# Optimization experiments

Hardware: AMD Instinct MI355X
Metric: run time of the kernel (lower is better)

The kernel has to match this reference:

```python
import jax, jax.numpy as jnp
import numpy as np

SELECTED_CLASS = 1  # matches init_kwargs


def _edt_sq(mask):
    """Exact squared Euclidean distance of each pixel to the nearest False pixel.
    Matches scipy.ndimage.distance_transform_edt(mask)**2 (2-pass separable,
    column scan + exact row-wise parabola minimization done brute-force in chunks).
    mask: (H, W) bool.
    """
    H, W = mask.shape
    BIG = np.float32(H + W)  # > any possible true distance, safe sentinel
    g = np.where(mask, BIG, np.float32(0.0)).astype(np.float32)
    for i in range(1, H):
        np.minimum(g[i], g[i - 1] + 1, out=g[i])
    for i in range(H - 2, -1, -1):
        np.minimum(g[i], g[i + 1] + 1, out=g[i])
    g2 = g * g  # (H, W) squared column distances
    k = np.arange(W, dtype=np.float32)
    d2 = np.empty((H, W), np.float32)
    CH = 64  # chunk of output columns to bound temp memory
    for j0 in range(0, W, CH):
        j = k[j0:j0 + CH]
        diff2 = (j[None, :] - k[:, None]) ** 2  # (W, Jc)
        d2[:, j0:j0 + CH] = (g2[:, :, None] + diff2[None]).min(axis=1)
    return d2


def _inner_boundary(mask):
    """skimage.segmentation.find_boundaries(mask, mode='inner'), connectivity=1:
    foreground pixels with at least one in-image 4-neighbor in background."""
    p = np.pad(mask, 1, constant_values=True)
    ero = p[1:-1, :-2] & p[1:-1, 2:] & p[:-2, 1:-1] & p[2:, 1:-1] & mask
    return mask & ~ero


def compute_sdf_np(y_true_sel):
    """Normalized signed distance map, faithful to BoundaryLoss.compute_sdf.
    y_true_sel: (B, 1, H, W) float; returns (B, 1, H, W) float32 in [-1, 1]."""
    masks = y_true_sel[:, 0].astype(bool)
    B, H, W = masks.shape
    out = np.zeros((B, 1, H, W), np.float32)
    for b in range(B):
        m = masks[b]
        if not m.any():
            continue  # original leaves zeros
        posdis = np.sqrt(_edt_sq(m))
        negdis = np.sqrt(_edt_sq(~m))
        sdf = (negdis - negdis.min()) / (negdis.max() - negdis.min()) \
            - (posdis - posdis.min()) / (posdis.max() - posdis.min())
        sdf[_inner_boundary(m)] = 0.0
        out[b, 0] = sdf
    return out


def setup_inputs():
    key = jax.random.key(0)
    k1, k2 = jax.random.split(key)
    B, C, H, W = 8, 4, 512, 512
    y_pred = jax.random.normal(k1, (B, C, H, W), dtype=jnp.float32)
    y_true = jax.random.randint(k2, (B, C, H, W), 0, 2).astype(jnp.float32)
    return {"y_pred": y_pred, "y_true": y_true}


def reference(y_pred, y_true):
    sel = SELECTED_CLASS
    # GT signed distance map (host-side, non-differentiable, as in the original
    # which round-trips through scipy on CPU): shape (B, 1, H, W)
    gt_sdf = jnp.asarray(compute_sdf_np(np.asarray(y_true[:, sel:sel + 1])))
    pc = jax.nn.sigmoid(y_pred)  # (B, C, H, W)
    # torch.einsum('bchw,bchw->bchw', pc, dc) with dc having c=1 broadcasts over C
    mult = pc * gt_sdf
    return mult.mean(axis=(1, 2, 3)).mean()
```

## Files before the change

### kernel.cpp

```cpp
#include <hip/hip_runtime.h>
#include <math.h>

#define B 8
#define C 4
#define H 512
#define W 512
#define SEL 1
#define BIGI 1024
#define NPIX (B*H*W)
#define CH 64
#define RC 8
#define TC 32
#define NSEG 16
#define LL 4
#define CINF 3000
#define G 8
#define NRU (B*H/G)
#define LOG2E 1.4426950408889634f

__global__ __launch_bounds__(512) void col_two_level(const float* __restrict__ ytrue,
                                                     unsigned short* __restrict__ gpkT,
                                                     unsigned* __restrict__ sumsD,
                                                     unsigned* __restrict__ sumsU) {
    __shared__ int sP[NSEG][TC + 1], sN[NSEG][TC + 1];
    __shared__ int sCP[NSEG][TC + 1], sCN[NSEG][TC + 1];

    int blk = blockIdx.x;
    int b   = blk >> 7;
    int rem = blk & 127;
    int jt  = rem >> 3;
    int rc  = rem & 7;
    int tid = threadIdx.x;
    int tx  = tid & (TC - 1);
    int ty  = tid >> 5;
    int j   = jt * TC + tx;
    int i0  = rc * CH + ty * LL;

    const float* m = ytrue + ((size_t)b * C + SEL) * H * W + j;
    int gfp[LL], gfn[LL];
    int pp = BIGI, pn = BIGI;
    #pragma unroll
    for (int r = 0; r < LL; ++r) {
        bool fg = (m[(size_t)(i0 + r) * W] != 0.0f);
        int vp = fg ? BIGI : 0;
        int vn = fg ? 0 : BIGI;
        vp = min(vp, pp + 1); gfp[r] = vp; pp = vp;
        vn = min(vn, pn + 1); gfn[r] = vn; pn = vn;
    }
    sP[ty][tx] = pp - ty * LL;
    sN[ty][tx] = pn - ty * LL;
    __syncthreads();

    int col = tid >> 4, seg = tid & 15;
    int wp = sP[seg][col], wn = sN[seg][col];
    #pragma unroll
    for (int d = 1; d < NSEG; d <<= 1) {
        int a1 = __shfl_up(wp, d, 16);
        int a2 = __shfl_up(wn, d, 16);
        if (seg >= d) { wp = min(wp, a1); wn = min(wn, a2); }
    }
    if (seg < NSEG - 1) {
        sCP[seg + 1][col] = seg * LL + wp;
        sCN[seg + 1][col] = seg * LL + wn;
    } else {
        int jj = jt * TC + col;
        sumsD[((size_t)(b * RC + rc)) * W + jj] =
            (unsigned)(seg * LL + wp) | ((unsigned)(seg * LL + wn) << 16);
    }
    if (seg == 0) { sCP[0][col] = BIGI; sCN[0][col] = BIGI; }
    __syncthreads();

    int cp = sCP[ty][tx], cn = sCN[ty][tx];
    int lbp = 1 << 20, lbn = 1 << 20;
    #pragma unroll
    for (int r = 0; r < LL; ++r) {
        int vp = min(gfp[r], cp + 1 + r); gfp[r] = vp; lbp = min(lbp, vp + r);
        int vn = min(gfn[r], cn + 1 + r); gfn[r] = vn; lbn = min(lbn, vn + r);
    }
    sP[ty][tx] = lbp + ty * LL;
    sN[ty][tx] = lbn + ty * LL;
    __syncthreads();

    int w2p = sP[seg][col], w2n = sN[seg][col];
    #pragma unroll
    for (int d = 1; d < NSEG; d <<= 1) {
        int a1 = __shfl_down(w2p, d, 16);
        int a2 = __shfl_down(w2n, d, 16);
        if (seg + d < NSEG) { w2p = min(w2p, a1); w2n = min(w2n, a2); }
    }
    if (seg > 0) {
        sCP[seg - 1][col] = w2p - seg * LL;
        sCN[seg - 1][col] = w2n - seg * LL;
    } else {
        int jj = jt * TC + col;
        sumsU[((size_t)(b * RC + rc)) * W + jj] =
            (unsigned)w2p | ((unsigned)w2n << 16);
    }
    if (seg == NSEG - 1) { sCP[NSEG - 1][col] = BIGI; sCN[NSEG - 1][col] = BIGI; }
    __syncthreads();

    int pbp = sCP[ty][tx], pbn = sCN[ty][tx];
    unsigned short g4[LL];
    #pragma unroll
    for (int r = LL - 1; r >= 0; --r) {
        int vp = min(gfp[r], pbp + 1); pbp = vp;
        int vn = min(gfn[r], pbn + 1); pbn = vn;
        int fg = (vn == 0) ? 1 : 0;
        int g2 = vp + vn;
        g4[r] = (unsigned short)((g2 << 1) | fg);
    }
    ushort4 pk; pk.x = g4[0]; pk.y = g4[1]; pk.z = g4[2]; pk.w = g4[3];
    *(ushort4*)(gpkT + (((size_t)b * (H / 4) + (i0 >> 2)) * W + j) * 4) = pk;
}

__global__ __launch_bounds__(512) void row_fused(const unsigned short* __restrict__ gpkT,
                                                 const unsigned* __restrict__ sumsD,
                                                 const unsigned* __restrict__ sumsU,
                                                 const float* __restrict__ ypred,
                                                 float* __restrict__ rowpart) {
    __shared__ float s1[G][W];
    __shared__ float sw[4][8];

    int blk = blockIdx.x;
    int b = blk >> 6;
    int g = blk & 63;
    int i0 = g * G;
    int rc = i0 >> 6;
    int j = threadIdx.x;

    const unsigned* sd = sumsD + (size_t)b * RC * W + j;
    const unsigned* su = sumsU + (size_t)b * RC * W + j;
    int Ap = CINF, An = CINF, Bp = CINF, Bn = CINF;
    #pragma unroll
    for (int q = 0; q < RC; ++q) {
        if (q < rc) {
            unsigned dv = sd[(size_t)q * W];
            int e = q * CH + CH - 1;
            Ap = min(Ap, (int)(dv & 0xFFFFu) - e);
            An = min(An, (int)(dv >> 16) - e);
        } else if (q > rc) {
            unsigned uv = su[(size_t)q * W];
            int s0 = q * CH;
            Bp = min(Bp, (int)(uv & 0xFFFFu) + s0);
            Bn = min(Bn, (int)(uv >> 16) + s0);
        }
    }

    float svr[G];
    #pragma unroll
    for (int h = 0; h < G; h += 4) {
        const ushort4 v4 = *(const ushort4*)(gpkT + (((size_t)b * (H / 4) + ((i0 + h) >> 2)) * W + j) * 4);
        unsigned short vv[4] = { v4.x, v4.y, v4.z, v4.w };
        #pragma unroll
        for (int r = 0; r < 4; ++r) {
            int ii = i0 + h + r;
            unsigned v = vv[r];
            int fg = v & 1;
            int gv = v >> 1;
            int gp = fg ? gv : 0;
            int gn = fg ? 0 : gv;
            gp = min(gp, min(Ap + ii, Bp - ii));
            gn = min(gn, min(An + ii, Bn - ii));
            int gg = gp + gn;
            float sv = (float)(gg * gg);
            sv = fg ? sv : -sv;
            svr[h + r] = sv;
            s1[h + r][j] = sv;
        }
    }

    float yv[G][C];
    #pragma unroll
    for (int r = 0; r < G; ++r) {
        const float* yp = ypred + ((size_t)b * C * H + i0 + r) * W + j;
        #pragma unroll
        for (int cc = 0; cc < C; ++cc) yv[r][cc] = yp[(size_t)cc * H * W];
    }
    __syncthreads();

    int jl1 = (j >= 1) ? j - 1 : j, jr1 = (j < W - 1) ? j + 1 : j;
    int jl2 = (j >= 2) ? j - 2 : j, jr2 = (j < W - 2) ? j + 2 : j;

    float mxp = 0.f, mxn = 0.f, A = 0.f, Bv = 0.f;
    #pragma unroll
    for (int r = 0; r < G; ++r) {
        float sv = svr[r];
        bool fg = (sv > 0.f);
        float sgn = fg ? 1.f : -1.f;
        float bq = fabsf(sv);
        float u1 = s1[r][jl1], u2 = s1[r][jr1], u3 = s1[r][jl2], u4 = s1[r][jr2];
        bq = fminf(bq, fmaxf(u1 * sgn, 0.f) + 1.f);
        bq = fminf(bq, fmaxf(u2 * sgn, 0.f) + 1.f);
        bq = fminf(bq, fmaxf(u3 * sgn, 0.f) + 4.f);
        bq = fminf(bq, fmaxf(u4 * sgn, 0.f) + 4.f);
        float r2 = 9.f, drr = 7.f;
        for (int rr = 3; rr < W; ++rr) {
            if (r2 >= bq) break;
            int jl = j - rr, jr = j + rr;
            if (jl >= 0) { float u = s1[r][jl]; bq = fminf(bq, fmaxf(u * sgn, 0.f) + r2); }
            if (jr < W)  { float u = s1[r][jr]; bq = fminf(bq, fmaxf(u * sgn, 0.f) + r2); }
            r2 += drr; drr += 2.f;
        }
        float d = __builtin_amdgcn_sqrtf(bq);
        bool bnd = fg && (bq == 1.0f);

        float s = __builtin_amdgcn_rcpf(1.0f + __builtin_amdgcn_exp2f(-yv[r][0] * LOG2E))
                + __builtin_amdgcn_rcpf(1.0f + __builtin_amdgcn_exp2f(-yv[r][1] * LOG2E))
                + __builtin_amdgcn_rcpf(1.0f + __builtin_amdgcn_exp2f(-yv[r][2] * LOG2E))
                + __builtin_amdgcn_rcpf(1.0f + __builtin_amdgcn_exp2f(-yv[r][3] * LOG2E));
        float se = bnd ? 0.f : s;
        mxp = fmaxf(mxp, fg ? bq : 0.f);
        mxn = fmaxf(mxn, fg ? 0.f : bq);
        A  += fg ? se * d : 0.f;
        Bv += fg ? 0.f : se * d;
    }

    for (int off = 32; off >= 1; off >>= 1) {
        mxp = fmaxf(mxp, __shfl_down(mxp, off));
        mxn = fmaxf(mxn, __shfl_down(mxn, off));
        A  += __shfl_down(A, off);
        Bv += __shfl_down(Bv, off);
    }
    int wave = threadIdx.x >> 6, lane = threadIdx.x & 63;
    if (lane == 0) { sw[0][wave] = mxp; sw[1][wave] = mxn; sw[2][wave] = A; sw[3][wave] = Bv; }
    __syncthreads();
    if (threadIdx.x == 0) {
        float a0 = sw[0][0], a1 = sw[1][0], a2 = sw[2][0], a3 = sw[3][0];
        #pragma unroll
        for (int w = 1; w < 8; ++w) {
            a0 = fmaxf(a0, sw[0][w]); a1 = fmaxf(a1, sw[1][w]);
            a2 += sw[2][w]; a3 += sw[3][w];
        }
        *(float4*)(rowpart + (size_t)blk * 4) = make_float4(a0, a1, a2, a3);
    }
}

__global__ __launch_bounds__(512) void batch_final(const float* __restrict__ rowpart,
                                                   float* __restrict__ out) {
    __shared__ double sacc[8];
    int bw = threadIdx.x >> 6;
    int lane = threadIdx.x & 63;
    const float4* rv = (const float4*)(rowpart + (size_t)bw * 64 * 4);
    float4 e0 = rv[lane];
    float mxp = e0.x, mxn = e0.y;
    float A = e0.z, Bv = e0.w;
    for (int off = 32; off >= 1; off >>= 1) {
        mxp = fmaxf(mxp, __shfl_down(mxp, off));
        mxn = fmaxf(mxn, __shfl_down(mxn, off));
        A  += __shfl_down(A, off);
        Bv += __shfl_down(Bv, off);
    }
    if (lane == 0) {
        float pmax = sqrtf(mxp), nmax = sqrtf(mxn);
        float invp = (pmax > 0.f) ? 1.0f / pmax : 0.0f;
        float invn = (nmax > 0.f) ? 1.0f / nmax : 0.0f;
        sacc[bw] = (pmax > 0.f) ? (double)(invn * Bv - invp * A) : 0.0;
    }
    __syncthreads();
    if (threadIdx.x == 0) {
        double tt = 0.0;
        #pragma unroll
        for (int q = 0; q < 8; ++q) tt += sacc[q];
        out[0] = (float)(tt / (double)((size_t)B * C * H * W));
    }
}

extern "C" void kernel_launch(void* const* d_in, const int* in_sizes, int n_in,
                              void* d_out, int out_size, void* d_ws, size_t ws_size,
                              hipStream_t stream) {
    const float* ypred = (const float*)d_in[0];
    const float* ytrue = (const float*)d_in[1];
    float* out = (float*)d_out;

    unsigned short* gpkT = (unsigned short*)d_ws;
    unsigned* sumsD = (unsigned*)(gpkT + NPIX);
    unsigned* sumsU = sumsD + (size_t)B * RC * W;
    float* rowpart = (float*)(sumsU + (size_t)B * RC * W);

    col_two_level<<<B * 16 * RC, 512, 0, stream>>>(ytrue, gpkT, sumsD, sumsU);
    row_fused<<<NRU, 512, 0, stream>>>(gpkT, sumsD, sumsU, ypred, rowpart);
    batch_final<<<1, 512, 0, stream>>>(rowpart, out);
}
```

Measured before the change: 24.19 us.

## Fuse final batch reduction into row kernel via atomics and last-block pattern

Drops the separate single-block batch_final kernel. Each row_fused block atomically accumulates fixed-point sums and integer maxima per batch, and the last block to finish (tracked by an atomic counter) computes the final scalar. The accumulators are zeroed inside the first kernel. This saves one kernel launch and its serial tail, at the cost of atomic contention and fixed-point quantization of the partial sums.

```diff
diff --git a/kernel.cpp b/kernel.cpp
--- a/kernel.cpp
+++ b/kernel.cpp
@@ -17,13 +17,22 @@
 #define G 8
 #define NRU (B*H/G)
 #define LOG2E 1.4426950408889634f
+#define SCALE_F 1048576.0f
+#define INV_SCALE (1.0 / 1048576.0)
 
 __global__ __launch_bounds__(512) void col_two_level(const float* __restrict__ ytrue,
                                                      unsigned short* __restrict__ gpkT,
                                                      unsigned* __restrict__ sumsD,
-                                                     unsigned* __restrict__ sumsU) {
+                                                     unsigned* __restrict__ sumsU,
+                                                     unsigned long long* __restrict__ parts,
+                                                     unsigned* __restrict__ cnt) {
     __shared__ int sP[NSEG][TC + 1], sN[NSEG][TC + 1];
     __shared__ int sCP[NSEG][TC + 1], sCN[NSEG][TC + 1];
+
+    if (blockIdx.x == 0) {
+        if (threadIdx.x < 64) parts[threadIdx.x] = 0ull;
+        if (threadIdx.x == 64) *cnt = 0u;
+    }
 
     int blk = blockIdx.x;
     int b   = blk >> 7;
@@ -117,16 +126,20 @@
                                                  const unsigned* __restrict__ sumsD,
                                                  const unsigned* __restrict__ sumsU,
                                                  const float* __restrict__ ypred,
-                                                 float* __restrict__ rowpart) {
+                                                 unsigned long long* __restrict__ parts,
+                                                 unsigned* __restrict__ cnt,
+                                                 float* __restrict__ out) {
     __shared__ float s1[G][W];
     __shared__ float sw[4][8];
+    __shared__ int lastFlag;
 
     int blk = blockIdx.x;
     int b = blk >> 6;
     int g = blk & 63;
     int i0 = g * G;
     int rc = i0 >> 6;
-    int j = threadIdx.x;
+    int tid = threadIdx.x;
+    int j = tid;
 
     const unsigned* sd = sumsD + (size_t)b * RC * W + j;
     const unsigned* su = sumsU + (size_t)b * RC * W + j;
@@ -221,47 +234,46 @@
         A  += __shfl_down(A, off);
         Bv += __shfl_down(Bv, off);
     }
-    int wave = threadIdx.x >> 6, lane = threadIdx.x & 63;
+    int wave = tid >> 6, lane = tid & 63;
     if (lane == 0) { sw[0][wave] = mxp; sw[1][wave] = mxn; sw[2][wave] = A; sw[3][wave] = Bv; }
     __syncthreads();
-    if (threadIdx.x == 0) {
+    if (tid == 0) {
         float a0 = sw[0][0], a1 = sw[1][0], a2 = sw[2][0], a3 = sw[3][0];
         #pragma unroll
         for (int w = 1; w < 8; ++w) {
             a0 = fmaxf(a0, sw[0][w]); a1 = fmaxf(a1, sw[1][w]);
             a2 += sw[2][w]; a3 += sw[3][w];
         }
-        *(float4*)(rowpart + (size_t)blk * 4) = make_float4(a0, a1, a2, a3);
-    }
-}
-
-__global__ __launch_bounds__(512) void batch_final(const float* __restrict__ rowpart,
-                                                   float* __restrict__ out) {
-    __shared__ double sacc[8];
-    int bw = threadIdx.x >> 6;
-    int lane = threadIdx.x & 63;
-    const float4* rv = (const float4*)(rowpart + (size_t)bw * 64 * 4);
-    float4 e0 = rv[lane];
-    float mxp = e0.x, mxn = e0.y;
-    float A = e0.z, Bv = e0.w;
-    for (int off = 32; off >= 1; off >>= 1) {
-        mxp = fmaxf(mxp, __shfl_down(mxp, off));
-        mxn = fmaxf(mxn, __shfl_down(mxn, off));
-        A  += __shfl_down(A, off);
-        Bv += __shfl_down(Bv, off);
-    }
-    if (lane == 0) {
-        float pmax = sqrtf(mxp), nmax = sqrtf(mxn);
-        float invp = (pmax > 0.f) ? 1.0f / pmax : 0.0f;
-        float invn = (nmax > 0.f) ? 1.0f / nmax : 0.0f;
-        sacc[bw] = (pmax > 0.f) ? (double)(invn * Bv - invp * A) : 0.0;
-    }
-    __syncthreads();
-    if (threadIdx.x == 0) {
-        double tt = 0.0;
-        #pragma unroll
-        for (int q = 0; q < 8; ++q) tt += sacc[q];
-        out[0] = (float)(tt / (double)((size_t)B * C * H * W));
+        unsigned long long* Pb = parts + (size_t)b * 8;
+        atomicAdd(Pb + 0, (unsigned long long)(a2 * SCALE_F + 0.5f));
+        atomicAdd(Pb + 1, (unsigned long long)(a3 * SCALE_F + 0.5f));
+        atomicMax(Pb + 2, (unsigned long long)(unsigned)a0);
+        atomicMax(Pb + 3, (unsigned long long)(unsigned)a1);
+        asm volatile("s_waitcnt vmcnt(0)" ::: "memory");
+        unsigned prev = atomicAdd(cnt, 1u);
+        lastFlag = (prev == (unsigned)(NRU - 1)) ? 1 : 0;
+    }
+    __syncthreads();
+
+    if (lastFlag) {
+        double contrib = 0.0;
+        if (tid < 8) {
+            unsigned long long* Pb = parts + (size_t)tid * 8;
+            unsigned long long uA = atomicAdd(Pb + 0, 0ull);
+            unsigned long long uB = atomicAdd(Pb + 1, 0ull);
+            unsigned long long mp = atomicAdd(Pb + 2, 0ull);
+            unsigned long long mn = atomicAdd(Pb + 3, 0ull);
+            double pmax = sqrt((double)mp), nmax = sqrt((double)mn);
+            double Ar = (double)uA * INV_SCALE;
+            double Br = (double)uB * INV_SCALE;
+            double invp = (pmax > 0.0) ? 1.0 / pmax : 0.0;
+            double invn = (nmax > 0.0) ? 1.0 / nmax : 0.0;
+            contrib = (pmax > 0.0) ? (invn * Br - invp * Ar) : 0.0;
+        }
+        contrib += __shfl_down(contrib, 4);
+        contrib += __shfl_down(contrib, 2);
+        contrib += __shfl_down(contrib, 1);
+        if (tid == 0) out[0] = (float)(contrib / (double)((size_t)B * C * H * W));
     }
 }
 
@@ -275,9 +287,9 @@
     unsigned short* gpkT = (unsigned short*)d_ws;
     unsigned* sumsD = (unsigned*)(gpkT + NPIX);
     unsigned* sumsU = sumsD + (size_t)B * RC * W;
-    float* rowpart = (float*)(sumsU + (size_t)B * RC * W);
-
-    col_two_level<<<B * 16 * RC, 512, 0, stream>>>(ytrue, gpkT, sumsD, sumsU);
-    row_fused<<<NRU, 512, 0, stream>>>(gpkT, sumsD, sumsU, ypred, rowpart);
-    batch_final<<<1, 512, 0, stream>>>(rowpart, out);
+    unsigned long long* parts = (unsigned long long*)(sumsU + (size_t)B * RC * W);
+    unsigned* cnt = (unsigned*)(parts + 64);
+
+    col_two_level<<<B * 16 * RC, 512, 0, stream>>>(ytrue, gpkT, sumsD, sumsU, parts, cnt);
+    row_fused<<<NRU, 512, 0, stream>>>(gpkT, sumsD, sumsU, ypred, parts, cnt, out);
 }
```

Result: slower. 26.48 us (+9.4%).
